# Performance work log

Hardware: AMD Instinct MI355X
Metric: run time of the kernel (lower is better)

Reference implementation:

```python
import jax, jax.numpy as jnp
import numpy as np

B, T, C = 4, 2048, 1024
H = 16
D = C // H  # head_dim = 64


def setup_inputs() -> dict:
    key = jax.random.key(0)
    ks = jax.random.split(key, 5)
    scale_in = 1.0 / np.sqrt(C)
    x = jax.random.normal(ks[0], (B, T, C), dtype=jnp.float32)
    w_qkv = jax.random.normal(ks[1], (C, 3 * C), dtype=jnp.float32) * scale_in
    b_qkv = jnp.zeros((3 * C,), dtype=jnp.float32)
    w_proj = jax.random.normal(ks[2], (C, C), dtype=jnp.float32) * scale_in
    b_proj = jnp.zeros((C,), dtype=jnp.float32)
    return {"x": x, "w_qkv": w_qkv, "b_qkv": b_qkv, "w_proj": w_proj, "b_proj": b_proj}


def reference(x, w_qkv, b_qkv, w_proj, b_proj):
    # fused QKV projection: [B,T,3C]
    qkv = x @ w_qkv + b_qkv
    q, k, v = jnp.split(qkv, 3, axis=-1)
    # [B,T,C] -> [B,H,T,D]
    q = q.reshape(B, T, H, D).transpose(0, 2, 1, 3)
    k = k.reshape(B, T, H, D).transpose(0, 2, 1, 3)
    v = v.reshape(B, T, H, D).transpose(0, 2, 1, 3)
    scale = 1.0 / np.sqrt(D)
    scores = jnp.einsum('bhqd,bhkd->bhqk', q, k) * scale  # [B,H,T,T]
    causal = jnp.tril(jnp.ones((T, T), dtype=bool))
    scores = jnp.where(causal, scores, jnp.finfo(scores.dtype).min)
    attn = jax.nn.softmax(scores, axis=-1)
    y = jnp.einsum('bhqk,bhkd->bhqd', attn, v)  # [B,H,T,D]
    y = y.transpose(0, 2, 1, 3).reshape(B, T, C)
    return y @ w_proj + b_proj
```

## Files before the change

### kernel.cpp

```cpp
#include <hip/hip_runtime.h>

typedef unsigned short u16;
typedef unsigned int u32;
typedef unsigned long long u64;
typedef __attribute__((ext_vector_type(8))) short s16x8;
typedef __attribute__((ext_vector_type(4))) float f32x4;

#if __has_builtin(__builtin_amdgcn_exp2f)
#define EXP2(x) __builtin_amdgcn_exp2f(x)
#else
#define EXP2(x) __expf((x) * 0.69314718f)
#endif

#if __has_builtin(__builtin_amdgcn_rcpf)
#define RCP(x) __builtin_amdgcn_rcpf(x)
#else
#define RCP(x) (1.0f / (x))
#endif

#define GLL(gp, lp) __builtin_amdgcn_global_load_lds(                         \
    (const __attribute__((address_space(1))) unsigned int*)(const void*)(gp), \
    (__attribute__((address_space(3))) unsigned int*)(void*)(lp), 16, 0, 0)

__device__ __forceinline__ u16 f2bf(float f) {
    union { float f; u32 u; } v; v.f = f;
    u32 r = v.u + 0x7FFF + ((v.u >> 16) & 1);
    return (u16)(r >> 16);
}

__device__ __forceinline__ u32 pack2_trunc(float a, float b) {
    union { float f; u32 u; } x, y; x.f = a; y.f = b;
    return (x.u >> 16) | (y.u & 0xFFFF0000u);
}

__device__ __forceinline__ float bf2f(u16 b) {
    union { u32 u; float f; } v; v.u = ((u32)b) << 16;
    return v.f;
}

__device__ __forceinline__ s16x8 scale_frag(s16x8 v, float s) {
    s16x8 o;
#pragma unroll
    for (int i = 0; i < 8; i++) o[i] = (short)f2bf(bf2f((u16)v[i]) * s);
    return o;
}

__global__ __launch_bounds__(256) void prep(const float* __restrict__ x,
                                            const float* __restrict__ w_qkv,
                                            const float* __restrict__ w_proj,
                                            u16* __restrict__ x_bf,
                                            u16* __restrict__ wqkvT,
                                            u16* __restrict__ wprojT) {
    int id = blockIdx.x, tid = threadIdx.x;
    if (id < 8192) {
        size_t i = ((size_t)id * 256 + tid) * 4;
        float4 f = *(const float4*)(x + i);
        u16 o[4] = { f2bf(f.x), f2bf(f.y), f2bf(f.z), f2bf(f.w) };
        *(u64*)(x_bf + i) = (u64)o[0] | ((u64)o[1] << 16) | ((u64)o[2] << 32) |
                            ((u64)o[3] << 48);
        return;
    }
    __shared__ float tile[32][33];
    const float* in; u16* out; int rows, cols, bx, by;
    if (id < 11264) {
        int blk = id - 8192; bx = blk % 96; by = blk / 96;
        in = w_qkv; out = wqkvT; rows = 1024; cols = 3072;
    } else {
        int blk = id - 11264; bx = blk & 31; by = blk >> 5;
        in = w_proj; out = wprojT; rows = 1024; cols = 1024;
    }
    int c0 = bx * 32, r0 = by * 32;
    int tx = tid & 31, ty = tid >> 5;
#pragma unroll
    for (int i = 0; i < 32; i += 8)
        tile[ty + i][tx] = in[(size_t)(r0 + ty + i) * cols + (c0 + tx)];
    __syncthreads();
#pragma unroll
    for (int i = 0; i < 32; i += 8)
        out[(size_t)(c0 + ty + i) * rows + (r0 + tx)] = f2bf(tile[tx][ty + i]);
}

template<int MODE>
__global__ __launch_bounds__(256, 4) void gemm_bt64(const u16* __restrict__ A,
                                                    const u16* __restrict__ BT,
                                                    const float* __restrict__ bias,
                                                    void* __restrict__ O1,
                                                    u16* __restrict__ vT,
                                                    int M, int N, int K) {
    __shared__ u16 SMEM[18432];
    u16* As = SMEM;
    u16* Bs = SMEM + 8192;
    int n0 = blockIdx.x * 128, m0 = blockIdx.y * 128;
    int tid = threadIdx.x, lane = tid & 63, w = tid >> 6;
    int row16 = lane & 15, quad = lane >> 4;
    int wm = (w >> 1) * 64, wn = (w & 1) * 64;
    f32x4 acc[4][4] = {};

    int lr = lane >> 3;
    int cswz = (lane & 7) ^ lr;
    const u16* Ag = A + (size_t)(m0 + w * 32 + lr) * K + cswz * 8;
    const u16* Bg = BT + (size_t)(n0 + w * 32 + lr) * K + cswz * 8;
    u16* Asl = As + (w * 32) * 64;
    u16* Bsl = Bs + (w * 32) * 64;

    for (int k0 = 0; k0 < K; k0 += 64) {
        __syncthreads();
#pragma unroll
        for (int j = 0; j < 4; j++) {
            GLL(Ag + k0 + (size_t)j * 8 * K, Asl + j * 8 * 64);
            GLL(Bg + k0 + (size_t)j * 8 * K, Bsl + j * 8 * 64);
        }
        __syncthreads();
#pragma unroll
        for (int kk = 0; kk < 2; kk++) {
            s16x8 af[4], bf[4];
#pragma unroll
            for (int mi = 0; mi < 4; mi++)
                af[mi] = *(const s16x8*)&As[(wm + mi * 16 + row16) * 64 +
                                            (((kk * 4 + quad) ^ (row16 & 7)) * 8)];
#pragma unroll
            for (int ni = 0; ni < 4; ni++)
                bf[ni] = *(const s16x8*)&Bs[(wn + ni * 16 + row16) * 64 +
                                            (((kk * 4 + quad) ^ (row16 & 7)) * 8)];
#pragma unroll
            for (int mi = 0; mi < 4; mi++)
#pragma unroll
                for (int ni = 0; ni < 4; ni++)
                    acc[mi][ni] = __builtin_amdgcn_mfma_f32_16x16x32_bf16(
                        af[mi], bf[ni], acc[mi][ni], 0, 0, 0);
        }
    }

    if (MODE == 0) {
        float* O = (float*)O1;
#pragma unroll
        for (int ni = 0; ni < 4; ni++) {
            int col = n0 + wn + ni * 16 + row16;
            float bv = bias[col];
#pragma unroll
            for (int mi = 0; mi < 4; mi++)
#pragma unroll
                for (int r = 0; r < 4; r++)
                    O[(size_t)(m0 + wm + mi * 16 + quad * 4 + r) * N + col] =
                        acc[mi][ni][r] + bv;
        }
    } else if (n0 < 2048) {
        u16* qk = (u16*)O1;
#pragma unroll
        for (int ni = 0; ni < 4; ni++) {
            int col = n0 + wn + ni * 16 + row16;
            float bv = bias[col];
#pragma unroll
            for (int mi = 0; mi < 4; mi++)
#pragma unroll
                for (int r = 0; r < 4; r++)
                    qk[(size_t)(m0 + wm + mi * 16 + quad * 4 + r) * 2048 + col] =
                        f2bf(acc[mi][ni][r] + bv);
        }
    } else {
        __syncthreads();
        u16* scr = SMEM + w * 64 * 72;
#pragma unroll
        for (int ni = 0; ni < 4; ni++) {
            float bv = bias[n0 + wn + ni * 16 + row16];
#pragma unroll
            for (int mi = 0; mi < 4; mi++)
#pragma unroll
                for (int r = 0; r < 4; r++)
                    scr[(ni * 16 + row16) * 72 + (mi * 16 + quad * 4 + r)] =
                        f2bf(acc[mi][ni][r] + bv);
        }
        __syncthreads();
        int r8 = lane >> 3, c8 = lane & 7;
        int vbase = (m0 >> 11) * 1024 + (n0 - 2048) + wn;
        int tb = (m0 & 2047) + wm;
#pragma unroll
        for (int it = 0; it < 8; it++) {
            s16x8 vv = *(const s16x8*)&scr[(it * 8 + r8) * 72 + c8 * 8];
            *(s16x8*)&vT[(size_t)(vbase + it * 8 + r8) * 2048 + tb + c8 * 8] = vv;
        }
    }
}

__global__ __launch_bounds__(128, 2) void attn_kernel(const u16* __restrict__ qk,
                                                      const u16* __restrict__ vT,
                                                      u16* __restrict__ y) {
    __shared__ u16 Kb[2][4096];
    __shared__ u16 Vb[2][4096];
    __shared__ u16 Ps[2][2048];

    int tid = threadIdx.x, lane = tid & 63, w = tid >> 6;
    int row16 = lane & 15, quad = lane >> 4;
    int id = blockIdx.x;
    int xcd = id & 7, slot = id >> 3;
    int pairi = slot >> 3;
    int bh = ((slot & 7) << 3) | xcd;
    int b = bh >> 4, h = bh & 15;
    const u16* qkb = qk + (size_t)b * 2048 * 2048;
    const u16* vtb = vT + ((size_t)(b * 1024) + h * 64) * 2048;

    int lr = lane >> 3, cswz = (lane & 7) ^ lr;
    const u16* Kg = qkb + (size_t)(w * 32 + lr) * 2048 + 1024 + h * 64 + cswz * 8;
    const u16* Vg = vtb + (size_t)(w * 32 + lr) * 2048 + cswz * 8;
    u16* Psw = Ps[w];
    int sw = row16 & 7;

    s16x8 ones;
#pragma unroll
    for (int i = 0; i < 8; i++) ones[i] = (short)0x3F80;
    const float qs = 0.125f * 1.44269504f;

    for (int half = 0; half < 2; half++) {
        int qt = half ? pairi : (31 - pairi);
        int q0 = qt * 64;
        int niter = qt + 1;
        int qw = q0 + w * 32;

        s16x8 qf[2][2];
#pragma unroll
        for (int mi = 0; mi < 2; mi++) {
            const u16* qp = qkb + (size_t)(qw + mi * 16 + row16) * 2048 + h * 64 + quad * 8;
            qf[mi][0] = scale_frag(*(const s16x8*)qp, qs);
            qf[mi][1] = scale_frag(*(const s16x8*)(qp + 32), qs);
        }

        f32x4 acc_o[2][4] = {};
        f32x4 acc_l[2] = {};

        __syncthreads();
#pragma unroll
        for (int j = 0; j < 4; j++) {
            GLL(Kg + (size_t)j * 8 * 2048, Kb[0] + w * 32 * 64 + j * 8 * 64);
            GLL(Vg + (size_t)j * 8 * 2048, Vb[0] + w * 32 * 64 + j * 8 * 64);
        }

        for (int kb = 0; kb < niter; kb++) {
            int cur = kb & 1;
            __syncthreads();
            if (kb + 1 < niter) {
                int k1 = (kb + 1) * 64;
#pragma unroll
                for (int j = 0; j < 4; j++) {
                    GLL(Kg + (size_t)(k1 + j * 8) * 2048, Kb[cur ^ 1] + w * 32 * 64 + j * 8 * 64);
                    GLL(Vg + k1 + (size_t)j * 8 * 2048, Vb[cur ^ 1] + w * 32 * 64 + j * 8 * 64);
                }
            }
            int k0 = kb * 64;
            if (k0 > qw + 31) continue;
            const u16* Kc = Kb[cur];
            const u16* Vc = Vb[cur];

            f32x4 sc[2][4];
#pragma unroll
            for (int nk = 0; nk < 4; nk++) {
                s16x8 kf0 = *(const s16x8*)&Kc[(nk * 16 + row16) * 64 + ((quad ^ sw) * 8)];
                s16x8 kf1 = *(const s16x8*)&Kc[(nk * 16 + row16) * 64 + (((4 + quad) ^ sw) * 8)];
#pragma unroll
                for (int mi = 0; mi < 2; mi++) {
                    f32x4 z = {};
                    z = __builtin_amdgcn_mfma_f32_16x16x32_bf16(kf0, qf[mi][0], z, 0, 0, 0);
                    z = __builtin_amdgcn_mfma_f32_16x16x32_bf16(kf1, qf[mi][1], z, 0, 0, 0);
                    sc[mi][nk] = z;
                }
            }
            if (k0 + 63 > qw) {
#pragma unroll
                for (int mi = 0; mi < 2; mi++) {
                    int qg = qw + mi * 16 + row16;
#pragma unroll
                    for (int nk = 0; nk < 4; nk++) {
                        int kbase = k0 + nk * 16 + quad * 4;
#pragma unroll
                        for (int r = 0; r < 4; r++)
                            if (kbase + r > qg) sc[mi][nk][r] = -__builtin_inff();
                    }
                }
            }
#pragma unroll
            for (int mi = 0; mi < 2; mi++)
#pragma unroll
                for (int nk = 0; nk < 4; nk++) {
                    float p0 = EXP2(sc[mi][nk][0]);
                    float p1 = EXP2(sc[mi][nk][1]);
                    float p2 = EXP2(sc[mi][nk][2]);
                    float p3 = EXP2(sc[mi][nk][3]);
                    u32 w0 = pack2_trunc(p0, p1);
                    u32 w1 = pack2_trunc(p2, p3);
                    int u = nk * 2 + (quad >> 1);
                    int eo = ((u ^ sw) * 8) + (quad & 1) * 4;
                    *(u64*)&Psw[mi * 1024 + row16 * 64 + eo] = (u64)w0 | ((u64)w1 << 32);
                }
#pragma unroll
            for (int kk = 0; kk < 2; kk++) {
                int co = ((kk * 4 + quad) ^ sw) * 8;
                s16x8 pf0 = *(const s16x8*)&Psw[row16 * 64 + co];
                s16x8 pf1 = *(const s16x8*)&Psw[1024 + row16 * 64 + co];
#pragma unroll
                for (int nd = 0; nd < 4; nd++) {
                    s16x8 vf = *(const s16x8*)&Vc[(nd * 16 + row16) * 64 + co];
                    acc_o[0][nd] = __builtin_amdgcn_mfma_f32_16x16x32_bf16(pf0, vf, acc_o[0][nd], 0, 0, 0);
                    acc_o[1][nd] = __builtin_amdgcn_mfma_f32_16x16x32_bf16(pf1, vf, acc_o[1][nd], 0, 0, 0);
                }
                acc_l[0] = __builtin_amdgcn_mfma_f32_16x16x32_bf16(pf0, ones, acc_l[0], 0, 0, 0);
                acc_l[1] = __builtin_amdgcn_mfma_f32_16x16x32_bf16(pf1, ones, acc_l[1], 0, 0, 0);
            }
        }

#pragma unroll
        for (int mi = 0; mi < 2; mi++) {
            int t0 = qw + mi * 16 + quad * 4;
#pragma unroll
            for (int r = 0; r < 4; r++) {
                float inv = RCP(acc_l[mi][r]);
#pragma unroll
                for (int nd = 0; nd < 4; nd++)
                    y[((size_t)b * 2048 + t0 + r) * 1024 + h * 64 + nd * 16 + row16] =
                        f2bf(acc_o[mi][nd][r] * inv);
            }
        }
    }
}

extern "C" void kernel_launch(void* const* d_in, const int* in_sizes, int n_in,
                              void* d_out, int out_size, void* d_ws, size_t ws_size,
                              hipStream_t stream) {
    const float* x      = (const float*)d_in[0];
    const float* w_qkv  = (const float*)d_in[1];
    const float* b_qkv  = (const float*)d_in[2];
    const float* w_proj = (const float*)d_in[3];
    const float* b_proj = (const float*)d_in[4];
    float* out = (float*)d_out;

    u16* ws     = (u16*)d_ws;
    u16* x_bf   = ws;
    u16* wqkvT  = x_bf  + (size_t)8192 * 1024;
    u16* wprojT = wqkvT + (size_t)3072 * 1024;
    u16* qkbuf  = wprojT + (size_t)1024 * 1024;
    u16* vT     = qkbuf + (size_t)8192 * 2048;
    u16* ybf    = vT    + (size_t)4096 * 2048;

    prep<<<dim3(12288), 256, 0, stream>>>(x, w_qkv, w_proj, x_bf, wqkvT, wprojT);
    gemm_bt64<1><<<dim3(24, 64), 256, 0, stream>>>(x_bf, wqkvT, b_qkv, (void*)qkbuf, vT, 8192, 3072, 1024);
    attn_kernel<<<dim3(1024), 128, 0, stream>>>(qkbuf, vT, ybf);
    gemm_bt64<0><<<dim3(8, 64), 256, 0, stream>>>(ybf, wprojT, b_proj, (void*)out, nullptr, 8192, 1024, 1024);
}
```

Measured before the change: 238.7 us.

## Restructure attention to 128-query tiles with V read directly from global

```diff
diff --git a/kernel.cpp b/kernel.cpp
--- a/kernel.cpp
+++ b/kernel.cpp
@@ -45,37 +45,24 @@
     return o;
 }
 
-__global__ __launch_bounds__(256) void prep(const float* __restrict__ x,
-                                            const float* __restrict__ w_qkv,
-                                            const float* __restrict__ w_proj,
-                                            u16* __restrict__ x_bf,
-                                            u16* __restrict__ wqkvT,
-                                            u16* __restrict__ wprojT) {
-    int id = blockIdx.x, tid = threadIdx.x;
-    if (id < 8192) {
-        size_t i = ((size_t)id * 256 + tid) * 4;
-        float4 f = *(const float4*)(x + i);
-        u16 o[4] = { f2bf(f.x), f2bf(f.y), f2bf(f.z), f2bf(f.w) };
-        *(u64*)(x_bf + i) = (u64)o[0] | ((u64)o[1] << 16) | ((u64)o[2] << 32) |
-                            ((u64)o[3] << 48);
-        return;
-    }
+__global__ __launch_bounds__(256) void cast_f32_bf16(const float* __restrict__ in,
+                                                     u16* __restrict__ out) {
+    size_t i = ((size_t)blockIdx.x * 256 + threadIdx.x) * 4;
+    float4 f = *(const float4*)(in + i);
+    u16 o[4] = { f2bf(f.x), f2bf(f.y), f2bf(f.z), f2bf(f.w) };
+    *(u64*)(out + i) = (u64)o[0] | ((u64)o[1] << 16) | ((u64)o[2] << 32) |
+                       ((u64)o[3] << 48);
+}
+
+__global__ __launch_bounds__(256) void transpose_cast(const float* __restrict__ in,
+                                                      u16* __restrict__ out,
+                                                      int rows, int cols) {
     __shared__ float tile[32][33];
-    const float* in; u16* out; int rows, cols, bx, by;
-    if (id < 11264) {
-        int blk = id - 8192; bx = blk % 96; by = blk / 96;
-        in = w_qkv; out = wqkvT; rows = 1024; cols = 3072;
-    } else {
-        int blk = id - 11264; bx = blk & 31; by = blk >> 5;
-        in = w_proj; out = wprojT; rows = 1024; cols = 1024;
-    }
-    int c0 = bx * 32, r0 = by * 32;
-    int tx = tid & 31, ty = tid >> 5;
-#pragma unroll
+    int c0 = blockIdx.x * 32, r0 = blockIdx.y * 32;
+    int tx = threadIdx.x, ty = threadIdx.y;
     for (int i = 0; i < 32; i += 8)
         tile[ty + i][tx] = in[(size_t)(r0 + ty + i) * cols + (c0 + tx)];
     __syncthreads();
-#pragma unroll
     for (int i = 0; i < 32; i += 8)
         out[(size_t)(c0 + ty + i) * rows + (r0 + tx)] = f2bf(tile[tx][ty + i]);
 }
@@ -182,26 +169,24 @@
     }
 }
 
-__global__ __launch_bounds__(128, 2) void attn_kernel(const u16* __restrict__ qk,
+__global__ __launch_bounds__(256, 4) void attn_kernel(const u16* __restrict__ qk,
                                                       const u16* __restrict__ vT,
                                                       u16* __restrict__ y) {
     __shared__ u16 Kb[2][4096];
-    __shared__ u16 Vb[2][4096];
-    __shared__ u16 Ps[2][2048];
+    __shared__ u16 Ps[4][2048];
 
     int tid = threadIdx.x, lane = tid & 63, w = tid >> 6;
     int row16 = lane & 15, quad = lane >> 4;
     int id = blockIdx.x;
     int xcd = id & 7, slot = id >> 3;
-    int pairi = slot >> 3;
+    int qt = 15 - (slot >> 3);
     int bh = ((slot & 7) << 3) | xcd;
     int b = bh >> 4, h = bh & 15;
     const u16* qkb = qk + (size_t)b * 2048 * 2048;
     const u16* vtb = vT + ((size_t)(b * 1024) + h * 64) * 2048;
 
     int lr = lane >> 3, cswz = (lane & 7) ^ lr;
-    const u16* Kg = qkb + (size_t)(w * 32 + lr) * 2048 + 1024 + h * 64 + cswz * 8;
-    const u16* Vg = vtb + (size_t)(w * 32 + lr) * 2048 + cswz * 8;
+    const u16* Kg = qkb + (size_t)(w * 16 + lr) * 2048 + 1024 + h * 64 + cswz * 8;
     u16* Psw = Ps[w];
     int sw = row16 & 7;
 
@@ -210,113 +195,115 @@
     for (int i = 0; i < 8; i++) ones[i] = (short)0x3F80;
     const float qs = 0.125f * 1.44269504f;
 
-    for (int half = 0; half < 2; half++) {
-        int qt = half ? pairi : (31 - pairi);
-        int q0 = qt * 64;
-        int niter = qt + 1;
-        int qw = q0 + w * 32;
-
-        s16x8 qf[2][2];
-#pragma unroll
-        for (int mi = 0; mi < 2; mi++) {
-            const u16* qp = qkb + (size_t)(qw + mi * 16 + row16) * 2048 + h * 64 + quad * 8;
-            qf[mi][0] = scale_frag(*(const s16x8*)qp, qs);
-            qf[mi][1] = scale_frag(*(const s16x8*)(qp + 32), qs);
-        }
-
-        f32x4 acc_o[2][4] = {};
-        f32x4 acc_l[2] = {};
-
-        __syncthreads();
-#pragma unroll
-        for (int j = 0; j < 4; j++) {
-            GLL(Kg + (size_t)j * 8 * 2048, Kb[0] + w * 32 * 64 + j * 8 * 64);
-            GLL(Vg + (size_t)j * 8 * 2048, Vb[0] + w * 32 * 64 + j * 8 * 64);
-        }
-
-        for (int kb = 0; kb < niter; kb++) {
-            int cur = kb & 1;
-            __syncthreads();
-            if (kb + 1 < niter) {
-                int k1 = (kb + 1) * 64;
-#pragma unroll
-                for (int j = 0; j < 4; j++) {
-                    GLL(Kg + (size_t)(k1 + j * 8) * 2048, Kb[cur ^ 1] + w * 32 * 64 + j * 8 * 64);
-                    GLL(Vg + k1 + (size_t)j * 8 * 2048, Vb[cur ^ 1] + w * 32 * 64 + j * 8 * 64);
+    int q0 = qt * 128;
+    int niter = 2 * qt + 2;
+    int qw = q0 + w * 32;
+
+    s16x8 qf[2][2];
+#pragma unroll
+    for (int mi = 0; mi < 2; mi++) {
+        const u16* qp = qkb + (size_t)(qw + mi * 16 + row16) * 2048 + h * 64 + quad * 8;
+        qf[mi][0] = scale_frag(*(const s16x8*)qp, qs);
+        qf[mi][1] = scale_frag(*(const s16x8*)(qp + 32), qs);
+    }
+
+    f32x4 acc_o[2][4] = {};
+    f32x4 acc_l[2] = {};
+
+#pragma unroll
+    for (int j = 0; j < 2; j++)
+        GLL(Kg + (size_t)j * 8 * 2048, Kb[0] + w * 16 * 64 + j * 8 * 64);
+
+    for (int kb = 0; kb < niter; kb++) {
+        int cur = kb & 1;
+        int k0 = kb * 64;
+        bool active = (k0 <= qw + 31);
+        __syncthreads();
+
+        s16x8 vf[8];
+        if (active) {
+#pragma unroll
+            for (int kk = 0; kk < 2; kk++)
+#pragma unroll
+                for (int nd = 0; nd < 4; nd++)
+                    vf[kk * 4 + nd] = *(const s16x8*)&vtb[(size_t)(nd * 16 + row16) * 2048 +
+                                                          k0 + kk * 32 + quad * 8];
+        }
+        if (kb + 1 < niter) {
+            int k1 = (kb + 1) * 64;
+#pragma unroll
+            for (int j = 0; j < 2; j++)
+                GLL(Kg + (size_t)(k1 + j * 8) * 2048, Kb[cur ^ 1] + w * 16 * 64 + j * 8 * 64);
+        }
+        if (!active) continue;
+        const u16* Kc = Kb[cur];
+
+        f32x4 sc[2][4];
+#pragma unroll
+        for (int nk = 0; nk < 4; nk++) {
+            s16x8 kf0 = *(const s16x8*)&Kc[(nk * 16 + row16) * 64 + ((quad ^ sw) * 8)];
+            s16x8 kf1 = *(const s16x8*)&Kc[(nk * 16 + row16) * 64 + (((4 + quad) ^ sw) * 8)];
+#pragma unroll
+            for (int mi = 0; mi < 2; mi++) {
+                f32x4 z = {};
+                z = __builtin_amdgcn_mfma_f32_16x16x32_bf16(kf0, qf[mi][0], z, 0, 0, 0);
+                z = __builtin_amdgcn_mfma_f32_16x16x32_bf16(kf1, qf[mi][1], z, 0, 0, 0);
+                sc[mi][nk] = z;
+            }
+        }
+        if (k0 + 63 > qw) {
+#pragma unroll
+            for (int mi = 0; mi < 2; mi++) {
+                int qg = qw + mi * 16 + row16;
+#pragma unroll
+                for (int nk = 0; nk < 4; nk++) {
+                    int kbase = k0 + nk * 16 + quad * 4;
+#pragma unroll
+                    for (int r = 0; r < 4; r++)
+                        if (kbase + r > qg) sc[mi][nk][r] = -__builtin_inff();
                 }
             }
-            int k0 = kb * 64;
-            if (k0 > qw + 31) continue;
-            const u16* Kc = Kb[cur];
-            const u16* Vc = Vb[cur];
-
-            f32x4 sc[2][4];
+        }
+#pragma unroll
+        for (int mi = 0; mi < 2; mi++)
 #pragma unroll
             for (int nk = 0; nk < 4; nk++) {
-                s16x8 kf0 = *(const s16x8*)&Kc[(nk * 16 + row16) * 64 + ((quad ^ sw) * 8)];
-                s16x8 kf1 = *(const s16x8*)&Kc[(nk * 16 + row16) * 64 + (((4 + quad) ^ sw) * 8)];
-#pragma unroll
-                for (int mi = 0; mi < 2; mi++) {
-                    f32x4 z = {};
-                    z = __builtin_amdgcn_mfma_f32_16x16x32_bf16(kf0, qf[mi][0], z, 0, 0, 0);
-                    z = __builtin_amdgcn_mfma_f32_16x16x32_bf16(kf1, qf[mi][1], z, 0, 0, 0);
-                    sc[mi][nk] = z;
-                }
+                float p0 = EXP2(sc[mi][nk][0]);
+                float p1 = EXP2(sc[mi][nk][1]);
+                float p2 = EXP2(sc[mi][nk][2]);
+                float p3 = EXP2(sc[mi][nk][3]);
+                u32 w0 = pack2_trunc(p0, p1);
+                u32 w1 = pack2_trunc(p2, p3);
+                int u = nk * 2 + (quad >> 1);
+                int eo = ((u ^ sw) * 8) + (quad & 1) * 4;
+                *(u64*)&Psw[mi * 1024 + row16 * 64 + eo] = (u64)w0 | ((u64)w1 << 32);
             }
-            if (k0 + 63 > qw) {
-#pragma unroll
-                for (int mi = 0; mi < 2; mi++) {
-                    int qg = qw + mi * 16 + row16;
-#pragma unroll
-                    for (int nk = 0; nk < 4; nk++) {
-                        int kbase = k0 + nk * 16 + quad * 4;
-#pragma unroll
-                        for (int r = 0; r < 4; r++)
-                            if (kbase + r > qg) sc[mi][nk][r] = -__builtin_inff();
-                    }
-                }
+#pragma unroll
+        for (int kk = 0; kk < 2; kk++) {
+            int co = ((kk * 4 + quad) ^ sw) * 8;
+            s16x8 pf0 = *(const s16x8*)&Psw[row16 * 64 + co];
+            s16x8 pf1 = *(const s16x8*)&Psw[1024 + row16 * 64 + co];
+#pragma unroll
+            for (int nd = 0; nd < 4; nd++) {
+                s16x8 vfr = vf[kk * 4 + nd];
+                acc_o[0][nd] = __builtin_amdgcn_mfma_f32_16x16x32_bf16(pf0, vfr, acc_o[0][nd], 0, 0, 0);
+                acc_o[1][nd] = __builtin_amdgcn_mfma_f32_16x16x32_bf16(pf1, vfr, acc_o[1][nd], 0, 0, 0);
             }
-#pragma unroll
-            for (int mi = 0; mi < 2; mi++)
-#pragma unroll
-                for (int nk = 0; nk < 4; nk++) {
-                    float p0 = EXP2(sc[mi][nk][0]);
-                    float p1 = EXP2(sc[mi][nk][1]);
-                    float p2 = EXP2(sc[mi][nk][2]);
-                    float p3 = EXP2(sc[mi][nk][3]);
-                    u32 w0 = pack2_trunc(p0, p1);
-                    u32 w1 = pack2_trunc(p2, p3);
-                    int u = nk * 2 + (quad >> 1);
-                    int eo = ((u ^ sw) * 8) + (quad & 1) * 4;
-                    *(u64*)&Psw[mi * 1024 + row16 * 64 + eo] = (u64)w0 | ((u64)w1 << 32);
-                }
-#pragma unroll
-            for (int kk = 0; kk < 2; kk++) {
-                int co = ((kk * 4 + quad) ^ sw) * 8;
-                s16x8 pf0 = *(const s16x8*)&Psw[row16 * 64 + co];
-                s16x8 pf1 = *(const s16x8*)&Psw[1024 + row16 * 64 + co];
-#pragma unroll
-                for (int nd = 0; nd < 4; nd++) {
-                    s16x8 vf = *(const s16x8*)&Vc[(nd * 16 + row16) * 64 + co];
-                    acc_o[0][nd] = __builtin_amdgcn_mfma_f32_16x16x32_bf16(pf0, vf, acc_o[0][nd], 0, 0, 0);
-                    acc_o[1][nd] = __builtin_amdgcn_mfma_f32_16x16x32_bf16(pf1, vf, acc_o[1][nd], 0, 0, 0);
-                }
-                acc_l[0] = __builtin_amdgcn_mfma_f32_16x16x32_bf16(pf0, ones, acc_l[0], 0, 0, 0);
-                acc_l[1] = __builtin_amdgcn_mfma_f32_16x16x32_bf16(pf1, ones, acc_l[1], 0, 0, 0);
-            }
-        }
-
-#pragma unroll
-        for (int mi = 0; mi < 2; mi++) {
-            int t0 = qw + mi * 16 + quad * 4;
-#pragma unroll
-            for (int r = 0; r < 4; r++) {
-                float inv = RCP(acc_l[mi][r]);
-#pragma unroll
-                for (int nd = 0; nd < 4; nd++)
-                    y[((size_t)b * 2048 + t0 + r) * 1024 + h * 64 + nd * 16 + row16] =
-                        f2bf(acc_o[mi][nd][r] * inv);
-            }
+            acc_l[0] = __builtin_amdgcn_mfma_f32_16x16x32_bf16(pf0, ones, acc_l[0], 0, 0, 0);
+            acc_l[1] = __builtin_amdgcn_mfma_f32_16x16x32_bf16(pf1, ones, acc_l[1], 0, 0, 0);
+        }
+    }
+
+#pragma unroll
+    for (int mi = 0; mi < 2; mi++) {
+        int t0 = qw + mi * 16 + quad * 4;
+#pragma unroll
+        for (int r = 0; r < 4; r++) {
+            float inv = RCP(acc_l[mi][r]);
+#pragma unroll
+            for (int nd = 0; nd < 4; nd++)
+                y[((size_t)b * 2048 + t0 + r) * 1024 + h * 64 + nd * 16 + row16] =
+                    f2bf(acc_o[mi][nd][r] * inv);
         }
     }
 }
@@ -339,8 +326,10 @@
     u16* vT     = qkbuf + (size_t)8192 * 2048;
     u16* ybf    = vT    + (size_t)4096 * 2048;
 
-    prep<<<dim3(12288), 256, 0, stream>>>(x, w_qkv, w_proj, x_bf, wqkvT, wprojT);
+    cast_f32_bf16<<<dim3(8192), 256, 0, stream>>>(x, x_bf);
+    transpose_cast<<<dim3(96, 32), dim3(32, 8), 0, stream>>>(w_qkv, wqkvT, 1024, 3072);
+    transpose_cast<<<dim3(32, 32), dim3(32, 8), 0, stream>>>(w_proj, wprojT, 1024, 1024);
     gemm_bt64<1><<<dim3(24, 64), 256, 0, stream>>>(x_bf, wqkvT, b_qkv, (void*)qkbuf, vT, 8192, 3072, 1024);
-    attn_kernel<<<dim3(1024), 128, 0, stream>>>(qkbuf, vT, ybf);
+    attn_kernel<<<dim3(1024), 256, 0, stream>>>(qkbuf, vT, ybf);
     gemm_bt64<0><<<dim3(8, 64), 256, 0, stream>>>(ybf, wprojT, b_proj, (void*)out, nullptr, 8192, 1024, 1024);
 }
```

Result: slower. 354.5 us (+48.5%).
